# Kernel tuning notes

Hardware: AMD Instinct MI355X
Metric: run time of the kernel (lower is better)

## Reference

```python
import jax, jax.numpy as jnp
import numpy as np

NUM_HOPS = 2
GAMMA = 0.8


def setup_inputs() -> dict:
    key = jax.random.key(0)
    ks = jax.random.split(key, 17)
    B, L, V, E, M, Mt, R = 8, 128, 50257, 768, 400, 800, 40
    W = 0.02  # init scale for learned params
    return {
        'hidden_states': jax.random.normal(ks[0], (B, L, E), jnp.float32),
        'wte': jax.random.normal(ks[1], (V, E), jnp.float32) * W,
        'rel_emb': jax.random.normal(ks[2], (R, E), jnp.float32) * W,
        'W_s': jax.random.normal(ks[3], (NUM_HOPS, E, E), jnp.float32) * W,
        'W_n': jax.random.normal(ks[4], (NUM_HOPS, E, E), jnp.float32) * W,
        'W_r': jax.random.normal(ks[5], (NUM_HOPS, E, E), jnp.float32) * W,
        'W_triple': jax.random.normal(ks[6], (E, 3 * E), jnp.float32) * W,
        'gate_w': jax.random.normal(ks[7], (E,), jnp.float32) * W,
        'gate_b': jnp.zeros((), jnp.float32),
        'concept_ids': jax.random.randint(ks[8], (B, M), 0, V),
        'relation_ids': jax.random.randint(ks[9], (B, Mt), 0, R),
        'head_idx': jax.random.randint(ks[10], (B, Mt), 0, M),
        'tail_idx': jax.random.randint(ks[11], (B, Mt), 0, M),
        'triple_labels': jax.random.randint(ks[12], (B, Mt), 0, 2),
        'distances': jax.random.randint(ks[13], (B, M), 0, 3),
        'vocab_map': jax.random.randint(ks[14], (V,), 0, M),
        'map_mask': jax.random.randint(ks[15], (V,), 0, 2),
    }


def _triple_encoder(wte, rel_emb, W_s, W_n, W_r, concept_ids, relation_ids, head_idx, tail_idx):
    concept_repr = wte[concept_ids]      # B,M,E
    rel_repr = rel_emb[relation_ids]     # B,Mt,E

    def gcn(cr, rr, h, t):               # per-batch CompGCN, faithful to torch loop
        M = cr.shape[0]
        ch, rh = cr, rr
        for l in range(NUM_HOPS):
            upd = jnp.zeros_like(cr)
            upd = upd.at[t].add(cr[h] - rr)   # scatter_add(o) + scatter_add(-rel)
            upd = upd.at[h].add(cr[t] - rr)
            cnt = jnp.zeros((M,), cr.dtype).at[t].add(1.0).at[h].add(1.0)
            upd = cr @ W_s[l].T + (upd @ W_n[l].T) / jnp.clip(cnt, 1.0, None)[:, None]
            ch = jax.nn.relu(upd)
            rh = rr @ W_r[l].T
        return ch, rh

    node, relh = jax.vmap(gcn)(concept_repr, rel_repr, head_idx, tail_idx)
    E = node.shape[-1]
    hi = jnp.broadcast_to(head_idx[:, :, None], head_idx.shape + (E,))
    ti = jnp.broadcast_to(tail_idx[:, :, None], tail_idx.shape + (E,))
    hrep = jnp.take_along_axis(node, hi, axis=1)
    trep = jnp.take_along_axis(node, ti, axis=1)
    return jnp.concatenate([hrep, relh, trep], axis=-1)  # B,Mt,3E


def _multi_hop(triple_prob, distances, head, tail):
    B, L, Mt = triple_prob.shape
    M = distances.shape[1]
    dt = triple_prob.dtype
    init_mask = jnp.broadcast_to((distances == 0).astype(dt)[:, None, :], (B, L, M))
    decay = (0.8 ** distances.astype(dt))[:, None, :]
    head_b = jnp.broadcast_to(head[:, None, :], (B, L, Mt))

    def scatter_mean(vals, t):  # vals: L,Mt  t: Mt -> L,M
        s = jnp.zeros((L, M), vals.dtype).at[:, t].add(vals)
        c = jnp.zeros((M,), vals.dtype).at[t].add(1.0)
        return s / jnp.clip(c, 1.0, None)

    node_score = init_mask
    total = init_mask * (-100000.0)
    for _ in range(NUM_HOPS):
        ths = jnp.take_along_axis(node_score, head_b, axis=2)  # B,L,Mt
        upd = ths * GAMMA + triple_prob
        node_score = jax.vmap(scatter_mean)(upd, tail)          # B,L,M
        total = total + node_score * decay
    return total


def reference(hidden_states, wte, rel_emb, W_s, W_n, W_r, W_triple, gate_w, gate_b,
              concept_ids, relation_ids, head_idx, tail_idx, triple_labels,
              distances, vocab_map, map_mask):
    triple_repr = _triple_encoder(wte, rel_emb, W_s, W_n, W_r,
                                  concept_ids, relation_ids, head_idx, tail_idx)
    lm_probs = jax.nn.softmax(hidden_states @ wte.T, axis=-1)            # B,L,V
    tl = triple_repr @ W_triple.T                                        # B,Mt,E
    triple_prob = jax.nn.sigmoid(jnp.einsum('ble,bme->blm', hidden_states, tl))
    triple_prob = triple_prob * (triple_labels != -1)[:, None, :].astype(triple_prob.dtype)
    scores = _multi_hop(triple_prob, distances, head_idx, tail_idx)      # B,L,M
    concept_probs = jax.nn.softmax(scores, axis=-1)
    cpv = concept_probs[:, :, vocab_map]                                 # gather into vocab: B,L,V
    cpv = cpv * (map_mask != 0)[None, None, :].astype(cpv.dtype)
    gate = jax.nn.sigmoid(hidden_states @ gate_w + gate_b)[..., None]    # B,L,1
    probs = gate * cpv + (1.0 - gate) * lm_probs
    return probs
```

## Files before the change

kernel.cpp:

```cpp
#include <hip/hip_runtime.h>
#include <stdint.h>

#define HB 8
#define HL 128
#define HV 50257
#define HE 768
#define HM 400
#define HMT 800
#define HBL (HB*HL)
#define NTILES 393
#define ELD 50272

typedef __attribute__((ext_vector_type(4))) float f32x4;
typedef __attribute__((ext_vector_type(8))) short bf16x8;
typedef unsigned short u16;

struct u16x4 { u16 x, y, z, w; };

__device__ __forceinline__ u16 f2bf(float x){
  union { float f; uint32_t u; } v; v.f = x;
  uint32_t r = v.u + 0x7fffu + ((v.u >> 16) & 1u);
  return (u16)(r >> 16);
}
__device__ __forceinline__ float bf2f(u16 b){
  union { uint32_t u; float f; } v; v.u = ((uint32_t)b) << 16;
  return v.f;
}
__device__ __forceinline__ void glds(const u16* g, const u16* l){
  __builtin_amdgcn_global_load_lds(
      (const __attribute__((address_space(1))) void*)g,
      (__attribute__((address_space(3))) void*)l, 16, 0, 0);
}

__global__ __launch_bounds__(256) void prep_k(const float* __restrict__ hs,
    const float* __restrict__ rel, const float* __restrict__ Wr1src,
    const float* __restrict__ Wt, const float* __restrict__ Ws1,
    const float* __restrict__ Wn1, const int* __restrict__ vmap,
    const int* __restrict__ mmask, const float* __restrict__ wte,
    u16* __restrict__ hid_b, u16* __restrict__ rel_b,
    u16* __restrict__ wr1, u16* __restrict__ wtT, u16* __restrict__ wcat,
    int* __restrict__ vmm, u16* __restrict__ wte_b){
  const int b = blockIdx.x, t = threadIdx.x;
  if (b >= 5456) {
    long i = (long)(b-5456)*256 + t;
    if (i < (long)HV*HE/4) {
      float4 x = ((const float4*)wte)[i];
      u16x4 y; y.x=f2bf(x.x); y.y=f2bf(x.y); y.z=f2bf(x.z); y.w=f2bf(x.w);
      ((u16x4*)wte_b)[i] = y;
    }
    return;
  }
  if (b < 768) {
    int i = b*256 + t;
    float4 x = ((const float4*)hs)[i];
    u16x4 y; y.x=f2bf(x.x); y.y=f2bf(x.y); y.z=f2bf(x.z); y.w=f2bf(x.w);
    ((u16x4*)hid_b)[i] = y;
  } else if (b < 798) {
    int i = (b-768)*256 + t;
    float4 x = ((const float4*)rel)[i];
    u16x4 y; y.x=f2bf(x.x); y.y=f2bf(x.y); y.z=f2bf(x.z); y.w=f2bf(x.w);
    ((u16x4*)rel_b)[i] = y;
  } else if (b < 1374) {
    int i = (b-798)*256 + t;
    float4 x = ((const float4*)Wr1src)[i];
    u16x4 y; y.x=f2bf(x.x); y.y=f2bf(x.y); y.z=f2bf(x.z); y.w=f2bf(x.w);
    ((u16x4*)wr1)[i] = y;
  } else if (b < 3102) {
    int g = (b-1374)*256 + t;
    int f = g / 192, r = g - f*192, e0 = r*4;
    u16x4 y;
    y.x = f2bf(Wt[(long)(e0+0)*2304 + f]);
    y.y = f2bf(Wt[(long)(e0+1)*2304 + f]);
    y.z = f2bf(Wt[(long)(e0+2)*2304 + f]);
    y.w = f2bf(Wt[(long)(e0+3)*2304 + f]);
    *(u16x4*)&wtT[(long)f*HE + e0] = y;
  } else if (b < 5406) {
    int i = (b-3102)*256 + t;
    int e = i / HE, k = i - e*HE;
    wcat[(long)e*(2*HE) + k]      = f2bf(Ws1[i]);
    wcat[(long)e*(2*HE) + HE + k] = f2bf(Wn1[i]);
  } else {
    int base = (b-5406)*1024 + t*4;
    #pragma unroll
    for (int i = 0; i < 4; ++i) {
      int c = base + i;
      if (c < HV) vmm[c] = mmask[c] ? vmap[c] : -1;
    }
  }
}

__global__ __launch_bounds__(256) void gcn_scatter_k(const float* __restrict__ wte,
    const float* __restrict__ rel, const int* __restrict__ cids,
    const int* __restrict__ rids, const int* __restrict__ head,
    const int* __restrict__ tail, u16* __restrict__ An){
  const int ch = blockIdx.x % 48;
  const int b  = blockIdx.x / 48;
  const int e0 = ch * 16;
  __shared__ float cw[HM][17];
  __shared__ float upd[HM][17];
  __shared__ float relc[40][17];
  __shared__ float cnt[HM];
  const int tid = threadIdx.x;

  for (int idx = tid; idx < HM*16; idx += 256) {
    int m = idx >> 4, e = idx & 15;
    cw[m][e] = wte[(long)cids[b*HM+m]*HE + e0 + e];
    upd[m][e] = 0.f;
  }
  for (int idx = tid; idx < 40*16; idx += 256) {
    int r = idx >> 4, e = idx & 15;
    relc[r][e] = rel[r*HE + e0 + e];
  }
  for (int m = tid; m < HM; m += 256) cnt[m] = 0.f;
  __syncthreads();

  for (int j = tid; j < HMT; j += 256) {
    int h = head[b*HMT+j], t = tail[b*HMT+j], r = rids[b*HMT+j];
    atomicAdd(&cnt[t], 1.f);
    atomicAdd(&cnt[h], 1.f);
    #pragma unroll
    for (int e = 0; e < 16; ++e) {
      float rv = relc[r][e];
      atomicAdd(&upd[t][e], cw[h][e] - rv);
      atomicAdd(&upd[h][e], cw[t][e] - rv);
    }
  }
  __syncthreads();

  for (int idx = tid; idx < HM*16; idx += 256) {
    int m = idx >> 4, e = idx & 15;
    float ic = 1.f / fmaxf(cnt[m], 1.f);
    u16* dst = An + ((long)b*HM + m) * (2*HE);
    dst[e0 + e]      = f2bf(cw[m][e]);
    dst[HE + e0 + e] = f2bf(upd[m][e] * ic);
  }
}

template<int ACT, int OUTBF16, int BIG, int DBUF>
__device__ __forceinline__ void gemm_core(
    const u16* __restrict__ Ab, const u16* __restrict__ Bb,
    void* __restrict__ Cout, float* __restrict__ rowpart,
    int Mdim, int Ndim, int Kdim, int lda, int ldb, int ldc,
    int mtile, int ntile, u16* AsmB, u16* BsmB)
{
  const int m0 = mtile * 128;
  const int n0 = ntile * 128;
  const int tid = threadIdx.x;
  const int lane = tid & 63;
  const int wid = tid >> 6;
  const int wr = wid >> 1, wc = wid & 1;
  const int srw = lane >> 3;
  const int sl  = lane & 7;

  f32x4 acc[4][4] = {};

  auto stage = [&](int buf, int k0) {
    u16* As = AsmB + buf*8192;
    u16* Bs = BsmB + buf*8192;
    #pragma unroll
    for (int i = 0; i < 4; ++i) {
      const int c = i*4 + wid;
      const int row = c*8 + srw;
      const int koff = k0 + ((sl ^ srw) * 8);
      int ra = m0 + row; if (ra > Mdim-1) ra = Mdim-1;
      glds(Ab + (long)ra * lda + koff, &As[c*512]);
      int rn = n0 + row; if (rn > Ndim-1) rn = Ndim-1;
      glds(Bb + (long)rn * ldb + koff, &Bs[c*512]);
    }
  };
  auto compute = [&](int buf) {
    const u16* As = AsmB + buf*8192;
    const u16* Bs = BsmB + buf*8192;
    #pragma unroll
    for (int kk = 0; kk < 2; ++kk) {
      bf16x8 af[4], bfr[4];
      #pragma unroll
      for (int mi = 0; mi < 4; ++mi) {
        const int R = wr*64 + mi*16 + (lane & 15);
        af[mi] = *(const bf16x8*)&As[R*64 + (((kk*4 + (lane>>4)) ^ (R & 7)) * 8)];
      }
      #pragma unroll
      for (int ni = 0; ni < 4; ++ni) {
        const int R = wc*64 + ni*16 + (lane & 15);
        bfr[ni] = *(const bf16x8*)&Bs[R*64 + (((kk*4 + (lane>>4)) ^ (R & 7)) * 8)];
      }
      #pragma unroll
      for (int mi = 0; mi < 4; ++mi)
        #pragma unroll
        for (int ni = 0; ni < 4; ++ni)
          acc[mi][ni] = __builtin_amdgcn_mfma_f32_16x16x32_bf16(af[mi], bfr[ni], acc[mi][ni], 0, 0, 0);
    }
  };

  const int NT = Kdim >> 6;
  if (DBUF) {
    stage(0, 0);
    __syncthreads();
    int cur = 0;
    for (int t = 0; t < NT; ++t) {
      if (t + 1 < NT) stage(cur ^ 1, (t + 1) << 6);
      compute(cur);
      __syncthreads();
      cur ^= 1;
    }
  } else {
    for (int t = 0; t < NT; ++t) {
      stage(0, t << 6);
      __syncthreads();
      compute(0);
      __syncthreads();
    }
  }

  const int cr0 = m0 + wr*64 + ((lane >> 4) * 4);
  const int cc0 = n0 + wc*64 + (lane & 15);

  if (BIG) {
    float* rs = (float*)AsmB;
    #pragma unroll
    for (int mi = 0; mi < 4; ++mi) {
      #pragma unroll
      for (int r = 0; r < 4; ++r) {
        const int rowi = cr0 + mi*16 + r;
        float s = 0.f;
        #pragma unroll
        for (int ni = 0; ni < 4; ++ni) {
          const int col = cc0 + ni*16;
          if (col < Ndim) {
            float e = __expf(acc[mi][ni][r]);
            if (OUTBF16) ((u16*)Cout)[(long)rowi*ELD + col] = f2bf(e);
            else        ((float*)Cout)[(long)rowi*HV + col] = e;
            s += e;
          }
        }
        s += __shfl_xor(s, 8); s += __shfl_xor(s, 4);
        s += __shfl_xor(s, 2); s += __shfl_xor(s, 1);
        if ((lane & 15) == 0)
          rs[wc*128 + wr*64 + mi*16 + ((lane >> 4) << 2) + r] = s;
      }
    }
    __syncthreads();
    if (tid < 128)
      rowpart[(long)(m0 + tid) * NTILES + ntile] = rs[tid] + rs[128 + tid];
    return;
  }

  #pragma unroll
  for (int mi = 0; mi < 4; ++mi) {
    #pragma unroll
    for (int ni = 0; ni < 4; ++ni) {
      const int col = cc0 + ni*16;
      if (col < Ndim) {
        #pragma unroll
        for (int r = 0; r < 4; ++r) {
          const int rowi = cr0 + mi*16 + r;
          if (rowi < Mdim) {
            float v = acc[mi][ni][r];
            if (ACT == 1) v = fmaxf(v, 0.f);
            if (OUTBF16) ((u16*)Cout)[(long)rowi*ldc + col] = f2bf(v);
            else        ((float*)Cout)[(long)rowi*ldc + col] = v;
          }
        }
      }
    }
  }
}

template<int EXPBF>
__global__ __launch_bounds__(256) void gemm_big(
    const u16* __restrict__ hid_b, const u16* __restrict__ wte_b,
    void* __restrict__ expl, float* __restrict__ rowpart)
{
  __shared__ alignas(16) u16 Asm[8192];
  __shared__ alignas(16) u16 Bsm[8192];
  const int wg = (blockIdx.x & 7) * NTILES + (blockIdx.x >> 3);
  gemm_core<0,EXPBF,1,0>(hid_b, wte_b, expl, rowpart,
      HBL, HV, HE, HE, HE, (EXPBF ? ELD : HV), wg & 7, wg >> 3, Asm, Bsm);
}

__global__ __launch_bounds__(256) void gemm_multi0(
    const u16* __restrict__ anode, const u16* __restrict__ wcat,
    u16* __restrict__ nodeb, const u16* __restrict__ rel_b,
    const u16* __restrict__ wr1, u16* __restrict__ relWr,
    const u16* __restrict__ hid_b, const u16* __restrict__ wtT,
    u16* __restrict__ hw)
{
  __shared__ alignas(16) u16 Asm[2*8192];
  __shared__ alignas(16) u16 Bsm[2*8192];
  const int q = blockIdx.x;
  if (q < 192) {
    const int z = q / 24, r = q - z*24;
    gemm_core<1,1,0,1>(anode + (long)z*HM*2*HE, wcat, nodeb + (long)z*HM*HE,
        nullptr, HM, HE, 2*HE, 2*HE, 2*HE, HE, r & 3, r >> 2, Asm, Bsm);
  } else if (q < 198) {
    gemm_core<0,1,0,1>(rel_b, wr1, relWr, nullptr,
        40, HE, HE, HE, HE, HE, 0, q - 192, Asm, Bsm);
  } else {
    const int u = q - 198;
    gemm_core<0,1,0,1>(hid_b, wtT, hw, nullptr,
        HBL, 3*HE, HE, HE, HE, 3*HE, u & 7, u >> 3, Asm, Bsm);
  }
}

__global__ __launch_bounds__(256) void gemm_multi1(
    const u16* __restrict__ hw, const u16* __restrict__ nodeb,
    const u16* __restrict__ relWr, float* __restrict__ scores)
{
  __shared__ alignas(16) u16 Asm[2*8192];
  __shared__ alignas(16) u16 Bsm[2*8192];
  const int q = blockIdx.x;
  if (q < 32) {
    const int z = q >> 2;
    gemm_core<0,0,0,1>(hw + (long)z*HL*(3*HE), nodeb + (long)z*HM*HE,
        scores + (long)z*HL*840, nullptr,
        HL, HM, HE, 3*HE, HE, 840, 0, q & 3, Asm, Bsm);
  } else if (q < 64) {
    const int z = (q - 32) >> 2;
    gemm_core<0,0,0,1>(hw + (long)z*HL*(3*HE) + 2*HE, nodeb + (long)z*HM*HE,
        scores + (long)z*HL*840 + HM, nullptr,
        HL, HM, HE, 3*HE, HE, 840, 0, (q - 32) & 3, Asm, Bsm);
  } else {
    gemm_core<0,0,0,1>(hw + HE, relWr, scores + 2*HM, nullptr,
        HBL, 40, HE, 3*HE, HE, 840, q - 64, 0, Asm, Bsm);
  }
}

__global__ __launch_bounds__(256) void multihop_k(const float* __restrict__ scores,
    const float* __restrict__ hs, const float* __restrict__ gw,
    const float* __restrict__ gb,
    const int* __restrict__ head, const int* __restrict__ tail,
    const int* __restrict__ rids, const int* __restrict__ labels,
    const int* __restrict__ dist, float* __restrict__ gatev,
    float* __restrict__ cprob){
  const int bl = blockIdx.x;
  const int b = bl >> 7;
  const int tid = threadIdx.x;
  const int lane = tid & 63, wid = tid >> 6;
  __shared__ float srow[840];
  __shared__ float tp[HMT];
  __shared__ float ns[HM], sacc[HM], tot[HM], invc[HM], dec[HM];
  __shared__ float red[16];
  __shared__ float gred[4];
  const int* hb = head + b*HMT;
  const int* tb = tail + b*HMT;
  const int* rb = rids + b*HMT;
  const int* lb = labels + b*HMT;
  const float* sr = scores + (long)bl * 840;

  float gs = 0.f;
  for (int e = tid; e < HE; e += 256) gs += hs[(long)bl*HE + e] * gw[e];
  for (int o = 32; o; o >>= 1) gs += __shfl_down(gs, o);
  if (lane == 0) gred[wid] = gs;

  for (int i = tid; i < 840; i += 256) srow[i] = sr[i];
  for (int m = tid; m < HM; m += 256) {
    int d = dist[b*HM + m];
    float im = (d == 0) ? 1.f : 0.f;
    ns[m] = im; tot[m] = im * -100000.f;
    dec[m] = (d == 0) ? 1.f : ((d == 1) ? 0.8f : 0.64f);
    sacc[m] = 0.f; invc[m] = 0.f;
  }
  __syncthreads();
  if (tid == 0)
    gatev[bl] = 1.f / (1.f + __expf(-(gred[0]+gred[1]+gred[2]+gred[3] + gb[0])));
  for (int j = tid; j < HMT; j += 256) {
    atomicAdd(&invc[tb[j]], 1.f);
    float x = srow[hb[j]] + srow[HM + tb[j]] + srow[2*HM + rb[j]];
    tp[j] = (lb[j] == -1) ? 0.f : 1.f / (1.f + __expf(-x));
  }
  __syncthreads();
  for (int m = tid; m < HM; m += 256) invc[m] = 1.f / fmaxf(invc[m], 1.f);
  __syncthreads();

  for (int hop = 0; hop < 2; ++hop) {
    for (int j = tid; j < HMT; j += 256) {
      float u = ns[hb[j]] * 0.8f + tp[j];
      atomicAdd(&sacc[tb[j]], u);
    }
    __syncthreads();
    for (int m = tid; m < HM; m += 256) {
      float v = sacc[m] * invc[m];
      ns[m] = v; tot[m] += v * dec[m]; sacc[m] = 0.f;
    }
    __syncthreads();
  }

  float lmx = -3.4e38f;
  for (int m = tid; m < HM; m += 256) lmx = fmaxf(lmx, tot[m]);
  for (int o = 32; o; o >>= 1) lmx = fmaxf(lmx, __shfl_down(lmx, o));
  if (lane == 0) red[wid] = lmx;
  __syncthreads();
  float gmx = fmaxf(fmaxf(red[0], red[1]), fmaxf(red[2], red[3]));
  float ls = 0.f;
  for (int m = tid; m < HM; m += 256) ls += __expf(tot[m] - gmx);
  for (int o = 32; o; o >>= 1) ls += __shfl_down(ls, o);
  if (lane == 0) red[8 + wid] = ls;
  __syncthreads();
  float inv = 1.f / (red[8] + red[9] + red[10] + red[11]);
  float* outrow = cprob + (long)bl * HM;
  for (int m = tid; m < HM; m += 256) outrow[m] = __expf(tot[m] - gmx) * inv;
}

template<int EXPBF>
__global__ __launch_bounds__(256) void finalize_k(const void* __restrict__ expl,
    const float* __restrict__ rowpart, const float* __restrict__ gatev,
    const float* __restrict__ cprob, const int* __restrict__ vmm,
    float* __restrict__ out){
  const int r = blockIdx.x / 13;
  const int ch = blockIdx.x - r*13;
  const int tid = threadIdx.x;
  __shared__ float red[4];
  __shared__ float cpl[HM];
  float s = 0.f;
  for (int t = tid; t < NTILES; t += 256) s += rowpart[r*NTILES + t];
  for (int o = 32; o; o >>= 1) s += __shfl_down(s, o);
  if ((tid & 63) == 0) red[tid >> 6] = s;
  const float g = gatev[r];
  for (int m = tid; m < HM; m += 256) cpl[m] = g * cprob[r*HM + m];
  __syncthreads();
  const float scale = (1.f - g) / (red[0] + red[1] + red[2] + red[3]);
  const u16* erb = (const u16*)expl + (long)r * ELD;
  const float* erf = (const float*)expl + (long)r * HV;
  float* orow = out + (long)r * HV;
  #pragma unroll
  for (int it = 0; it < 2; ++it) {
    const int c = ch*4096 + it*2048 + tid*8;
    if (c + 8 <= HV) {
      float e[8];
      if (EXPBF) {
        bf16x8 v = *(const bf16x8*)&erb[c];
        #pragma unroll
        for (int i = 0; i < 8; ++i) e[i] = bf2f((u16)v[i]);
      } else {
        float4 a = *(const float4*)&erf[c];
        float4 b2 = *(const float4*)&erf[c+4];
        e[0]=a.x; e[1]=a.y; e[2]=a.z; e[3]=a.w;
        e[4]=b2.x; e[5]=b2.y; e[6]=b2.z; e[7]=b2.w;
      }
      int4 v0 = *(const int4*)&vmm[c];
      int4 v1 = *(const int4*)&vmm[c+4];
      const int ix[8] = {v0.x, v0.y, v0.z, v0.w, v1.x, v1.y, v1.z, v1.w};
      float o8[8];
      #pragma unroll
      for (int i = 0; i < 8; ++i)
        o8[i] = (ix[i] >= 0 ? cpl[ix[i]] : 0.f) + scale * e[i];
      *(float4*)&orow[c]   = make_float4(o8[0], o8[1], o8[2], o8[3]);
      *(float4*)&orow[c+4] = make_float4(o8[4], o8[5], o8[6], o8[7]);
    } else if (c < HV) {
      for (int i = 0; i < 8 && c + i < HV; ++i) {
        float e = EXPBF ? bf2f(((const u16*)expl)[(long)r*ELD + c + i]) : erf[c+i];
        int ix = vmm[c+i];
        orow[c+i] = (ix >= 0 ? cpl[ix] : 0.f) + scale * e;
      }
    }
  }
}

extern "C" void kernel_launch(void* const* d_in, const int* in_sizes, int n_in,
                              void* d_out, int out_size, void* d_ws, size_t ws_size,
                              hipStream_t stream)
{
  const float* hs   = (const float*)d_in[0];
  const float* wte  = (const float*)d_in[1];
  const float* rel  = (const float*)d_in[2];
  const float* Ws   = (const float*)d_in[3];
  const float* Wn   = (const float*)d_in[4];
  const float* Wr   = (const float*)d_in[5];
  const float* Wt   = (const float*)d_in[6];
  const float* gw   = (const float*)d_in[7];
  const float* gb   = (const float*)d_in[8];
  const int* cids   = (const int*)d_in[9];
  const int* rids   = (const int*)d_in[10];
  const int* head   = (const int*)d_in[11];
  const int* tail   = (const int*)d_in[12];
  const int* labels = (const int*)d_in[13];
  const int* dist   = (const int*)d_in[14];
  const int* vmap   = (const int*)d_in[15];
  const int* mmask  = (const int*)d_in[16];
  float* out = (float*)d_out;

  char* ws = (char*)d_ws;
  size_t o = 0;
  auto alloc = [&](size_t bytes) -> char* {
    char* p = ws + o; o = (o + bytes + 255) & ~(size_t)255; return p;
  };
  u16* wte_b     = (u16*)alloc((size_t)HV*HE*2);
  u16* hid_b     = (u16*)alloc((size_t)HBL*HE*2);
  float* cprob   = (float*)alloc((size_t)HBL*HM*4);
  float* rowpart = (float*)alloc((size_t)HBL*NTILES*4);
  float* gatev   = (float*)alloc(HBL*4);
  int* vmm       = (int*)alloc((size_t)HV*4);
  float* scores  = (float*)alloc((size_t)HBL*840*4);

  const bool bigws = ws_size >= (size_t)196*1024*1024;
  u16* expl = (u16*)(ws + o);
  u16* wcat  = (u16*)alloc((size_t)HE*2*HE*2);
  u16* wr1   = (u16*)alloc((size_t)HE*HE*2);
  u16* wtT   = (u16*)alloc((size_t)3*HE*HE*2);
  u16* rel_b = (u16*)alloc((size_t)40*HE*2);
  u16* anode = (u16*)alloc((size_t)HB*HM*2*HE*2);
  u16* nodeb = (u16*)alloc((size_t)HB*HM*HE*2);
  u16* relWr = (u16*)alloc((size_t)40*HE*2);
  u16* hw    = (u16*)alloc((size_t)HBL*3*HE*2);
  (void)in_sizes; (void)n_in; (void)out_size;

  prep_k<<<5456 + 37693, 256, 0, stream>>>(hs, rel, Wr + (size_t)HE*HE, Wt,
      Ws + (size_t)HE*HE, Wn + (size_t)HE*HE, vmap, mmask, wte,
      hid_b, rel_b, wr1, wtT, wcat, vmm, wte_b);

  gcn_scatter_k<<<HB*48, 256, 0, stream>>>(wte, rel, cids, rids, head, tail, anode);

  gemm_multi0<<<342, 256, 0, stream>>>(anode, wcat, nodeb, rel_b, wr1, relWr,
      hid_b, wtT, hw);
  gemm_multi1<<<72, 256, 0, stream>>>(hw, nodeb, relWr, scores);

  multihop_k<<<HBL, 256, 0, stream>>>(scores, hs, gw, gb, head, tail, rids,
      labels, dist, gatev, cprob);

  if (bigws) {
    gemm_big<1><<<3144, 256, 0, stream>>>(hid_b, wte_b, expl, rowpart);
    finalize_k<1><<<HBL*13, 256, 0, stream>>>(expl, rowpart, gatev, cprob,
        vmm, out);
  } else {
    gemm_big<0><<<3144, 256, 0, stream>>>(hid_b, wte_b, out, rowpart);
    finalize_k<0><<<HBL*13, 256, 0, stream>>>(out, rowpart, gatev, cprob,
        vmm, out);
  }
}
```

Baseline: 457.6 us.

## Spread wte bf16 conversion across the small GCN kernels to overlap work

After: 398.1 us. 13.0% less time.

```diff
diff --git a/kernel.cpp b/kernel.cpp
--- a/kernel.cpp
+++ b/kernel.cpp
@@ -10,6 +10,7 @@
 #define HBL (HB*HL)
 #define NTILES 393
 #define ELD 50272
+#define WTE_F4 ((long)HV*HE/4)
 
 typedef __attribute__((ext_vector_type(4))) float f32x4;
 typedef __attribute__((ext_vector_type(8))) short bf16x8;
@@ -31,25 +32,27 @@
       (const __attribute__((address_space(1))) void*)g,
       (__attribute__((address_space(3))) void*)l, 16, 0, 0);
 }
+__device__ __forceinline__ void cvt_slice(const float* __restrict__ src,
+    u16* __restrict__ dst, long lo4, long n4, int relb, int nb){
+  long i = lo4 + (long)relb*256 + threadIdx.x;
+  const long end = lo4 + n4;
+  const long stride = (long)nb*256;
+  for (; i < end; i += stride) {
+    float4 x = ((const float4*)src)[i];
+    u16x4 y; y.x=f2bf(x.x); y.y=f2bf(x.y); y.z=f2bf(x.z); y.w=f2bf(x.w);
+    ((u16x4*)dst)[i] = y;
+  }
+}
 
 __global__ __launch_bounds__(256) void prep_k(const float* __restrict__ hs,
     const float* __restrict__ rel, const float* __restrict__ Wr1src,
     const float* __restrict__ Wt, const float* __restrict__ Ws1,
     const float* __restrict__ Wn1, const int* __restrict__ vmap,
-    const int* __restrict__ mmask, const float* __restrict__ wte,
+    const int* __restrict__ mmask,
     u16* __restrict__ hid_b, u16* __restrict__ rel_b,
     u16* __restrict__ wr1, u16* __restrict__ wtT, u16* __restrict__ wcat,
-    int* __restrict__ vmm, u16* __restrict__ wte_b){
+    int* __restrict__ vmm){
   const int b = blockIdx.x, t = threadIdx.x;
-  if (b >= 5456) {
-    long i = (long)(b-5456)*256 + t;
-    if (i < (long)HV*HE/4) {
-      float4 x = ((const float4*)wte)[i];
-      u16x4 y; y.x=f2bf(x.x); y.y=f2bf(x.y); y.z=f2bf(x.z); y.w=f2bf(x.w);
-      ((u16x4*)wte_b)[i] = y;
-    }
-    return;
-  }
   if (b < 768) {
     int i = b*256 + t;
     float4 x = ((const float4*)hs)[i];
@@ -92,7 +95,12 @@
 __global__ __launch_bounds__(256) void gcn_scatter_k(const float* __restrict__ wte,
     const float* __restrict__ rel, const int* __restrict__ cids,
     const int* __restrict__ rids, const int* __restrict__ head,
-    const int* __restrict__ tail, u16* __restrict__ An){
+    const int* __restrict__ tail, u16* __restrict__ An,
+    u16* __restrict__ wte_b){
+  if (blockIdx.x >= 384) {
+    cvt_slice(wte, wte_b, 0, 3145728L, blockIdx.x - 384, 3072);
+    return;
+  }
   const int ch = blockIdx.x % 48;
   const int b  = blockIdx.x / 48;
   const int e0 = ch * 16;
@@ -269,13 +277,14 @@
 template<int EXPBF>
 __global__ __launch_bounds__(256) void gemm_big(
     const u16* __restrict__ hid_b, const u16* __restrict__ wte_b,
-    void* __restrict__ expl, float* __restrict__ rowpart)
+    void* __restrict__ expl, float* __restrict__ rowpart,
+    int Mdim, int Ndim, int Kdim, int lda, int ldb, int ldc)
 {
   __shared__ alignas(16) u16 Asm[8192];
   __shared__ alignas(16) u16 Bsm[8192];
   const int wg = (blockIdx.x & 7) * NTILES + (blockIdx.x >> 3);
   gemm_core<0,EXPBF,1,0>(hid_b, wte_b, expl, rowpart,
-      HBL, HV, HE, HE, HE, (EXPBF ? ELD : HV), wg & 7, wg >> 3, Asm, Bsm);
+      Mdim, Ndim, Kdim, lda, ldb, ldc, wg & 7, wg >> 3, Asm, Bsm);
 }
 
 __global__ __launch_bounds__(256) void gemm_multi0(
@@ -283,8 +292,13 @@
     u16* __restrict__ nodeb, const u16* __restrict__ rel_b,
     const u16* __restrict__ wr1, u16* __restrict__ relWr,
     const u16* __restrict__ hid_b, const u16* __restrict__ wtT,
-    u16* __restrict__ hw)
+    u16* __restrict__ hw, const float* __restrict__ wte,
+    u16* __restrict__ wte_b)
 {
+  if (blockIdx.x >= 342) {
+    cvt_slice(wte, wte_b, 3145728L, 4194304L, blockIdx.x - 342, 4096);
+    return;
+  }
   __shared__ alignas(16) u16 Asm[2*8192];
   __shared__ alignas(16) u16 Bsm[2*8192];
   const int q = blockIdx.x;
@@ -304,8 +318,13 @@
 
 __global__ __launch_bounds__(256) void gemm_multi1(
     const u16* __restrict__ hw, const u16* __restrict__ nodeb,
-    const u16* __restrict__ relWr, float* __restrict__ scores)
+    const u16* __restrict__ relWr, float* __restrict__ scores,
+    const float* __restrict__ wte, u16* __restrict__ wte_b)
 {
+  if (blockIdx.x >= 72) {
+    cvt_slice(wte, wte_b, 7340032L, 1048576L, blockIdx.x - 72, 1024);
+    return;
+  }
   __shared__ alignas(16) u16 Asm[2*8192];
   __shared__ alignas(16) u16 Bsm[2*8192];
   const int q = blockIdx.x;
@@ -331,7 +350,12 @@
     const int* __restrict__ head, const int* __restrict__ tail,
     const int* __restrict__ rids, const int* __restrict__ labels,
     const int* __restrict__ dist, float* __restrict__ gatev,
-    float* __restrict__ cprob){
+    float* __restrict__ cprob, const float* __restrict__ wte,
+    u16* __restrict__ wte_b){
+  if (blockIdx.x >= HBL) {
+    cvt_slice(wte, wte_b, 8388608L, WTE_F4 - 8388608L, blockIdx.x - HBL, 1280);
+    return;
+  }
   const int bl = blockIdx.x;
   const int b = bl >> 7;
   const int tid = threadIdx.x;
@@ -504,25 +528,29 @@
   u16* hw    = (u16*)alloc((size_t)HBL*3*HE*2);
   (void)in_sizes; (void)n_in; (void)out_size;
 
-  prep_k<<<5456 + 37693, 256, 0, stream>>>(hs, rel, Wr + (size_t)HE*HE, Wt,
-      Ws + (size_t)HE*HE, Wn + (size_t)HE*HE, vmap, mmask, wte,
-      hid_b, rel_b, wr1, wtT, wcat, vmm, wte_b);
-
-  gcn_scatter_k<<<HB*48, 256, 0, stream>>>(wte, rel, cids, rids, head, tail, anode);
-
-  gemm_multi0<<<342, 256, 0, stream>>>(anode, wcat, nodeb, rel_b, wr1, relWr,
-      hid_b, wtT, hw);
-  gemm_multi1<<<72, 256, 0, stream>>>(hw, nodeb, relWr, scores);
-
-  multihop_k<<<HBL, 256, 0, stream>>>(scores, hs, gw, gb, head, tail, rids,
-      labels, dist, gatev, cprob);
+  prep_k<<<5456, 256, 0, stream>>>(hs, rel, Wr + (size_t)HE*HE, Wt,
+      Ws + (size_t)HE*HE, Wn + (size_t)HE*HE, vmap, mmask,
+      hid_b, rel_b, wr1, wtT, wcat, vmm);
+
+  gcn_scatter_k<<<384 + 3072, 256, 0, stream>>>(wte, rel, cids, rids, head,
+      tail, anode, wte_b);
+
+  gemm_multi0<<<342 + 4096, 256, 0, stream>>>(anode, wcat, nodeb, rel_b, wr1,
+      relWr, hid_b, wtT, hw, wte, wte_b);
+  gemm_multi1<<<72 + 1024, 256, 0, stream>>>(hw, nodeb, relWr, scores,
+      wte, wte_b);
+
+  multihop_k<<<HBL + 1280, 256, 0, stream>>>(scores, hs, gw, gb, head, tail,
+      rids, labels, dist, gatev, cprob, wte, wte_b);
 
   if (bigws) {
-    gemm_big<1><<<3144, 256, 0, stream>>>(hid_b, wte_b, expl, rowpart);
+    gemm_big<1><<<3144, 256, 0, stream>>>(hid_b, wte_b, expl, rowpart,
+        HBL, HV, HE, HE, HE, ELD);
     finalize_k<1><<<HBL*13, 256, 0, stream>>>(expl, rowpart, gatev, cprob,
         vmm, out);
   } else {
-    gemm_big<0><<<3144, 256, 0, stream>>>(hid_b, wte_b, out, rowpart);
+    gemm_big<0><<<3144, 256, 0, stream>>>(hid_b, wte_b, out, rowpart,
+        HBL, HV, HE, HE, HE, HV);
     finalize_k<0><<<HBL*13, 256, 0, stream>>>(out, rowpart, gatev, cprob,
         vmm, out);
   }
```
